# Kernel tuning notes

Hardware: AMD Instinct MI355X
Metric: run time of the kernel (lower is better)

## Reference

```python
import jax, jax.numpy as jnp
import numpy as np

C = 1024  # channel dim
T = 2048  # max context / actual seq len
B = 8

def setup_inputs() -> dict:
    key = jax.random.key(0)
    k1, k2, k3 = jax.random.split(key, 3)
    x = jax.random.normal(k1, (B, T, C), dtype=jnp.float32)
    # torch nn.Linear(C, 3C, bias=False): y = x @ W.T, W shape [3C, C].
    # We store the pre-transposed [C, 3C] / [C, C] matrices for clean matmuls.
    scale = 1.0 / np.sqrt(C)
    Wqkv = jax.random.normal(k2, (C, 3 * C), dtype=jnp.float32) * scale
    Wproj = jax.random.normal(k3, (C, C), dtype=jnp.float32) * scale
    return {"x": x, "Wqkv": Wqkv, "Wproj": Wproj}

def reference(x, Wqkv, Wproj):
    t = x.shape[1]
    qkv = x @ Wqkv                      # [B, t, 3C]
    q, k, v = jnp.split(qkv, 3, axis=-1)  # each [B, t, C]
    w = jnp.einsum('btc,bsc->bts', q, k) * (C ** -0.5)  # [B, t, t]
    causal = jnp.triu(jnp.ones((t, t), dtype=bool), k=1)
    w = jnp.where(causal, -jnp.inf, w)
    a = jax.nn.softmax(w, axis=-1)      # [B, t, t]
    out = jnp.einsum('bts,bsc->btc', a, v)  # [B, t, C]
    return out @ Wproj
```

## Files before the change

### kernel.cpp

```cpp
#include <hip/hip_runtime.h>

typedef unsigned short u16;
typedef __attribute__((ext_vector_type(8))) short bf16x8;
typedef __attribute__((ext_vector_type(4))) float f32x4;

__device__ __forceinline__ u16 f2bf(float f) {
    unsigned u = __float_as_uint(f);
    u += 0x7fffu + ((u >> 16) & 1u);
    return (u16)(u >> 16);
}

__device__ __forceinline__ void g2l16(const void* g, void* l) {
    __builtin_amdgcn_global_load_lds((const __attribute__((address_space(1))) void*)g,
                                     (__attribute__((address_space(3))) void*)l, 16, 0, 0);
}

#define SPACK_ELEMS 2228224LL

#define BM 128
#define BN 128
#define BK 64

template <bool OUT_BF16>
__global__ __launch_bounds__(256, 4) void gemm_bt(
    const u16* __restrict__ A, const u16* __restrict__ B, void* __restrict__ Cout,
    int K, int lda, int ldb, int ldc,
    long long sA, long long sB, long long sC,
    float alpha, int mode)
{
    int bx, by;
    const int bz = blockIdx.z;
    if (mode == 1) {
        int l = blockIdx.x;
        by = (int)((sqrtf(8.f * (float)l + 1.f) - 1.f) * 0.5f);
        while ((by + 1) * (by + 2) / 2 <= l) ++by;
        while (by * (by + 1) / 2 > l) --by;
        bx = l - by * (by + 1) / 2;
    } else if (mode == 2) {
        bx = blockIdx.x; by = (int)gridDim.y - 1 - (int)blockIdx.y;
    } else {
        bx = blockIdx.x; by = blockIdx.y;
    }
    int Keff = K;
    if (mode == 2) { int cap = (by + 1) * BM; if (cap < Keff) Keff = cap; }

    __shared__ alignas(16) u16 As[BM * BK];
    __shared__ alignas(16) u16 Bs[BN * BK];

    const int tid  = threadIdx.x;
    const int wave = tid >> 6, lane = tid & 63;
    const int wm = wave >> 1, wn = wave & 1;
    const int q = lane >> 4, r = lane & 15;

    const long long Pby = 16384LL * (by * (by + 1) / 2);

    const u16* Ab;
    int lda_e = lda;
    if (mode == 2) {
        lda_e = 2 * (by + 1) * BM;
        Ab = A + sA * bz + 2 * Pby;
    } else {
        Ab = A + sA * bz + (size_t)(by * BM) * lda_e;
    }
    const u16* Bb = B + sB * bz + (size_t)(bx * BN) * ldb;

    const u16* ap[4]; const u16* bp[4]; int sb[4];
#pragma unroll
    for (int j = 0; j < 4; ++j) {
        int s   = (wave * 4 + j) * 64 + lane;
        int row = s >> 3;
        int cc  = (s & 7) ^ (row & 7);
        ap[j] = Ab + (size_t)row * lda_e + cc * 8;
        bp[j] = Bb + (size_t)row * ldb + cc * 8;
        sb[j] = (wave * 4 + j) * 64;
    }

    f32x4 acc[4][4] = {};

    const int kiters = Keff / BK;
    for (int kt = 0; kt < kiters; ++kt) {
#pragma unroll
        for (int j = 0; j < 4; ++j) { g2l16(ap[j], As + (size_t)sb[j] * 8); ap[j] += BK; }
#pragma unroll
        for (int j = 0; j < 4; ++j) { g2l16(bp[j], Bs + (size_t)sb[j] * 8); bp[j] += BK; }
        __syncthreads();
#pragma unroll
        for (int ks = 0; ks < 2; ++ks) {
            bf16x8 af[4], bfv[4];
#pragma unroll
            for (int i = 0; i < 4; ++i) {
                int mr = wm * 64 + i * 16 + r;
                int cc = (ks * 4 + q) ^ (mr & 7);
                af[i] = *(const bf16x8*)(As + mr * BK + cc * 8);
            }
#pragma unroll
            for (int i = 0; i < 4; ++i) {
                int nr = wn * 64 + i * 16 + r;
                int cc = (ks * 4 + q) ^ (nr & 7);
                bfv[i] = *(const bf16x8*)(Bs + nr * BK + cc * 8);
            }
#pragma unroll
            for (int i = 0; i < 4; ++i)
#pragma unroll
                for (int jn = 0; jn < 4; ++jn)
                    acc[i][jn] = __builtin_amdgcn_mfma_f32_16x16x32_bf16(
                        af[i], bfv[jn], acc[i][jn], 0, 0, 0);
        }
        __syncthreads();
    }

    if (mode == 1) {
        float* Cp = (float*)Cout + sC * bz + Pby;
        const int ldrow = (by + 1) * BM;
#pragma unroll
        for (int i = 0; i < 4; ++i) {
            int lr = wm * 64 + i * 16 + q * 4;
#pragma unroll
            for (int jn = 0; jn < 4; ++jn) {
                int col = bx * BN + wn * 64 + jn * 16 + r;
#pragma unroll
                for (int rr = 0; rr < 4; ++rr)
                    Cp[(size_t)(lr + rr) * ldrow + col] = acc[i][jn][rr] * alpha;
            }
        }
    } else if constexpr (OUT_BF16) {
        u16* Cp = (u16*)Cout + sC * bz;
#pragma unroll
        for (int i = 0; i < 4; ++i) {
            int rowb = by * BM + wm * 64 + i * 16 + q * 4;
#pragma unroll
            for (int jn = 0; jn < 4; ++jn) {
                int col = bx * BN + wn * 64 + jn * 16 + r;
#pragma unroll
                for (int rr = 0; rr < 4; ++rr)
                    Cp[(size_t)(rowb + rr) * ldc + col] = f2bf(acc[i][jn][rr] * alpha);
            }
        }
    } else {
        float* Cp = (float*)Cout + sC * bz;
#pragma unroll
        for (int i = 0; i < 4; ++i) {
            int rowb = by * BM + wm * 64 + i * 16 + q * 4;
#pragma unroll
            for (int jn = 0; jn < 4; ++jn) {
                int col = bx * BN + wn * 64 + jn * 16 + r;
#pragma unroll
                for (int rr = 0; rr < 4; ++rr)
                    Cp[(size_t)(rowb + rr) * ldc + col] = acc[i][jn][rr] * alpha;
            }
        }
    }
}

__global__ void cast_f32_bf16(const float4* __restrict__ in, ushort4* __restrict__ out) {
    int i = blockIdx.x * 256 + threadIdx.x;
    float4 f = in[i];
    ushort4 o;
    o.x = f2bf(f.x); o.y = f2bf(f.y); o.z = f2bf(f.z); o.w = f2bf(f.w);
    out[i] = o;
}

__global__ void transpose_cast_f32(const float* __restrict__ in, u16* __restrict__ out,
                                   int R, int Cc) {
    __shared__ u16 tile[32][33];
    int tx = threadIdx.x, ty = threadIdx.y;
    int c0 = blockIdx.x * 32, r0 = blockIdx.y * 32;
#pragma unroll
    for (int k = 0; k < 4; ++k)
        tile[ty + k * 8][tx] = f2bf(in[(size_t)(r0 + ty + k * 8) * Cc + c0 + tx]);
    __syncthreads();
#pragma unroll
    for (int k = 0; k < 4; ++k)
        out[(size_t)(c0 + ty + k * 8) * R + r0 + tx] = tile[tx][ty + k * 8];
}

__global__ __launch_bounds__(256) void softmax_causal_packed(
    float* __restrict__ S, long long sS)
{
    const int wave = threadIdx.x >> 6, lane = threadIdx.x & 63;
    const int t = blockIdx.x * 4 + wave;
    const int by = t >> 7, lr = t & 127;
    const int L = (by + 1) << 7;
    float* row = S + (long long)blockIdx.y * sS
               + 16384LL * (by * (by + 1) / 2) + (size_t)lr * L;
    const int n = t + 1;
    const int nit = (L + 255) >> 8;

    float v[32];
    float m = -1e30f;
    for (int it = 0; it < nit; ++it) {
        int c = it * 64 + lane;
        int e = c * 4;
        float4 f = make_float4(-1e30f, -1e30f, -1e30f, -1e30f);
        if (e < n) f = ((const float4*)row)[c];
        v[it * 4 + 0] = (e + 0 < n) ? f.x : -1e30f;
        v[it * 4 + 1] = (e + 1 < n) ? f.y : -1e30f;
        v[it * 4 + 2] = (e + 2 < n) ? f.z : -1e30f;
        v[it * 4 + 3] = (e + 3 < n) ? f.w : -1e30f;
        m = fmaxf(m, fmaxf(fmaxf(v[it * 4 + 0], v[it * 4 + 1]),
                           fmaxf(v[it * 4 + 2], v[it * 4 + 3])));
    }
    for (int off = 32; off > 0; off >>= 1) m = fmaxf(m, __shfl_xor(m, off));

    float s = 0.f;
    for (int it = 0; it < nit; ++it) {
#pragma unroll
        for (int j = 0; j < 4; ++j) {
            v[it * 4 + j] = __expf(v[it * 4 + j] - m);
            s += v[it * 4 + j];
        }
    }
    for (int off = 32; off > 0; off >>= 1) s += __shfl_xor(s, off);
    float inv = 1.f / s;

    u16* orow = (u16*)row;
    for (int it = 0; it < nit; ++it) {
        int c = it * 64 + lane;
        if (c * 4 < L) {
            ushort4 o;
            o.x = f2bf(v[it * 4 + 0] * inv);
            o.y = f2bf(v[it * 4 + 1] * inv);
            o.z = f2bf(v[it * 4 + 2] * inv);
            o.w = f2bf(v[it * 4 + 3] * inv);
            ((ushort4*)orow)[c] = o;
        }
    }
}

extern "C" void kernel_launch(void* const* d_in, const int* in_sizes, int n_in,
                              void* d_out, int out_size, void* d_ws, size_t ws_size,
                              hipStream_t stream)
{
    const float* x     = (const float*)d_in[0];
    const float* Wqkv  = (const float*)d_in[1];
    const float* Wproj = (const float*)d_in[2];
    float* out = (float*)d_out;

    const int Bb = 8, T = 2048, C1 = 1024, C3 = 3072;

    char* ws = (char*)d_ws;
    u16*  xb     = (u16*)(ws);
    u16*  VWpT   = (u16*)(ws);
    u16*  WqkvT  = (u16*)(ws +  33554432ULL);
    u16*  WprojT = (u16*)(ws +  39845888ULL);
    u16*  qkvb   = (u16*)(ws +  41943040ULL);
    float* Sbuf  = (float*)(ws + 142606336ULL);

    const unsigned long long sbytes = SPACK_ELEMS * 4ULL;
    int zc = 1;
    if      (ws_size >= 142606336ULL + 8ULL * sbytes) zc = 8;
    else if (ws_size >= 142606336ULL + 4ULL * sbytes) zc = 4;
    else if (ws_size >= 142606336ULL + 2ULL * sbytes) zc = 2;

    cast_f32_bf16<<<16384, 256, 0, stream>>>((const float4*)x, (ushort4*)xb);

    transpose_cast_f32<<<dim3(96, 32), dim3(32, 8), 0, stream>>>(Wqkv,  WqkvT,  C1, C3);
    transpose_cast_f32<<<dim3(32, 32), dim3(32, 8), 0, stream>>>(Wproj, WprojT, C1, C1);

    gemm_bt<true><<<dim3(24, 128, 1), 256, 0, stream>>>(
        xb, WqkvT, qkvb, C1, C1, C1, C3, 0, 0, 0, 1.0f, 0);

    gemm_bt<true><<<dim3(16, 8, 8), 256, 0, stream>>>(
        WprojT, qkvb + 2 * C1, VWpT, C1, C1, C3, T,
        0, (long long)T * C3, (long long)C1 * T, 1.0f, 0);

    for (int i = 0; i < Bb; i += zc) {
        const u16* qb   = qkvb + (long long)i * T * C3;
        const u16* kb   = qb + C1;
        const u16* vwpb = VWpT + (long long)i * C1 * T;
        float* ob = out + (long long)i * T * C1;

        gemm_bt<false><<<dim3(136, 1, zc), 256, 0, stream>>>(
            qb, kb, Sbuf, C1, C3, C3, 0,
            (long long)T * C3, (long long)T * C3, SPACK_ELEMS,
            0.03125f, 1);

        softmax_causal_packed<<<dim3(T / 4, zc), 256, 0, stream>>>(
            Sbuf, SPACK_ELEMS);

        gemm_bt<false><<<dim3(8, 16, zc), 256, 0, stream>>>(
            (const u16*)Sbuf, vwpb, ob, T, 0, T, C1,
            2LL * SPACK_ELEMS, (long long)C1 * T, (long long)T * C1,
            1.0f, 2);
    }

    (void)in_sizes; (void)n_in; (void)out_size;
}
```

Baseline: 431.6 us.

## Add 256x256-tile 8-wave pipelined GEMM for QKV and V·Wproj projections

Adds a new bf16 GEMM kernel with 256x256 output tiles, 512 threads, double-buffered direct global-to-LDS loads, a fine-grained interleave of LDS reads, global staging and MFMA with explicit waitcnt/barrier control, and setprio around MFMA bursts. The QKV projection and the V×Wproj precompute now use it instead of the 128x128 kernel, aiming for more reuse per loaded byte and better overlap of loads with matrix math. Fewer blocks (768 and 256) may underfill the GPU's CUs, and the heavy manual scheduling depends on the compiler honouring the ordering and on register pressure at 2 blocks per CU.

```diff
diff --git a/kernel.cpp b/kernel.cpp
--- a/kernel.cpp
+++ b/kernel.cpp
@@ -152,6 +152,152 @@
     }
 }
 
+#define GBM 256
+#define GBN 256
+#define GBK 64
+
+__global__ __launch_bounds__(512, 2) void gemm256_bt(
+    const u16* __restrict__ A, const u16* __restrict__ B, u16* __restrict__ Cout,
+    int K, int lda, int ldb, int ldc,
+    long long sA, long long sB, long long sC)
+{
+    const int bx = blockIdx.x, by = blockIdx.y, bz = blockIdx.z;
+
+    __shared__ alignas(16) u16 As[2][GBM * GBK];
+    __shared__ alignas(16) u16 Bs[2][GBN * GBK];
+
+    const int tid  = threadIdx.x;
+    const int wave = tid >> 6, lane = tid & 63;
+    const int wm = wave >> 2, wn = wave & 3;
+    const int q = lane >> 4, r = lane & 15;
+
+    const u16* Ab = A + sA * bz + (size_t)(by * GBM) * lda;
+    const u16* Bb = B + sB * bz + (size_t)(bx * GBN) * ldb;
+
+    const u16* ap[2][2]; const u16* bp[2][2];
+#pragma unroll
+    for (int h = 0; h < 2; ++h)
+#pragma unroll
+        for (int l = 0; l < 2; ++l) {
+            int s   = l * 512 + tid;
+            int row = h * 128 + (s >> 3);
+            int cc  = (s & 7) ^ (row & 7);
+            ap[h][l] = Ab + (size_t)row * lda + cc * 8;
+            bp[h][l] = Bb + (size_t)row * ldb + cc * 8;
+        }
+
+#define STAGE_A(buf, h)                                                        \
+    { g2l16(ap[h][0], &As[buf][((h) * 1024 + 0 * 512 + wave * 64) * 8]);       \
+      ap[h][0] += GBK;                                                         \
+      g2l16(ap[h][1], &As[buf][((h) * 1024 + 1 * 512 + wave * 64) * 8]);       \
+      ap[h][1] += GBK; }
+#define STAGE_B(buf, h)                                                        \
+    { g2l16(bp[h][0], &Bs[buf][((h) * 1024 + 0 * 512 + wave * 64) * 8]);       \
+      bp[h][0] += GBK;                                                         \
+      g2l16(bp[h][1], &Bs[buf][((h) * 1024 + 1 * 512 + wave * 64) * 8]);       \
+      bp[h][1] += GBK; }
+
+    bf16x8 a[4][2], b0[2][2], b1[2][2];
+    f32x4 acc[8][4] = {};
+
+#define G_LDA(mh, buf)                                                         \
+    { _Pragma("unroll") for (int m = 0; m < 4; ++m)                            \
+      _Pragma("unroll") for (int ks = 0; ks < 2; ++ks) {                       \
+          int rw = wm * 128 + (mh) * 64 + m * 16 + r;                          \
+          int cc = (ks * 4 + q) ^ (r & 7);                                     \
+          a[m][ks] = *(const bf16x8*)(&As[buf][rw * GBK + cc * 8]);            \
+      } }
+#define G_LDB(nh, breg, buf)                                                   \
+    { _Pragma("unroll") for (int n = 0; n < 2; ++n)                            \
+      _Pragma("unroll") for (int ks = 0; ks < 2; ++ks) {                       \
+          int rw = wn * 64 + (nh) * 32 + n * 16 + r;                           \
+          int cc = (ks * 4 + q) ^ (r & 7);                                     \
+          breg[n][ks] = *(const bf16x8*)(&Bs[buf][rw * GBK + cc * 8]);         \
+      } }
+#define MFMA16(mh, nh, breg)                                                   \
+    { __builtin_amdgcn_s_setprio(1);                                          \
+      _Pragma("unroll") for (int m = 0; m < 4; ++m)                            \
+      _Pragma("unroll") for (int n = 0; n < 2; ++n)                            \
+      _Pragma("unroll") for (int ks = 0; ks < 2; ++ks)                         \
+          acc[(mh) * 4 + m][(nh) * 2 + n] =                                    \
+              __builtin_amdgcn_mfma_f32_16x16x32_bf16(                         \
+                  a[m][ks], breg[n][ks], acc[(mh) * 4 + m][(nh) * 2 + n],      \
+                  0, 0, 0);                                                    \
+      __builtin_amdgcn_s_setprio(0); }
+
+#define BARR                                                                   \
+    { asm volatile("" ::: "memory");                                           \
+      __builtin_amdgcn_s_barrier();                                            \
+      asm volatile("" ::: "memory"); }
+#define WLGKM asm volatile("s_waitcnt lgkmcnt(0)" ::: "memory")
+#define WVM4 asm volatile("s_waitcnt vmcnt(4)" ::: "memory")
+#define WVM0 asm volatile("s_waitcnt vmcnt(0)" ::: "memory")
+
+    STAGE_B(0, 0); STAGE_B(0, 1);
+    STAGE_A(0, 0); STAGE_A(0, 1);
+    STAGE_B(1, 0); STAGE_B(1, 1);
+    WVM4;
+    BARR;
+
+    const int niter = K / (2 * GBK);
+    for (int i = 0; i < niter - 1; ++i) {
+        G_LDA(0, 0); G_LDB(0, b0, 0); STAGE_A(1, 0);
+        BARR; WLGKM; MFMA16(0, 0, b0); BARR;
+        G_LDB(1, b1, 0); STAGE_A(1, 1);
+        BARR; WLGKM; MFMA16(0, 1, b1); BARR;
+        G_LDA(1, 0); STAGE_B(0, 0);
+        BARR; WLGKM; MFMA16(1, 0, b0); BARR;
+        STAGE_B(0, 1); WVM4;
+        BARR; MFMA16(1, 1, b1); BARR;
+        G_LDA(0, 1); G_LDB(0, b0, 1); STAGE_A(0, 0);
+        BARR; WLGKM; MFMA16(0, 0, b0); BARR;
+        G_LDB(1, b1, 1); STAGE_A(0, 1);
+        BARR; WLGKM; MFMA16(0, 1, b1); BARR;
+        G_LDA(1, 1); STAGE_B(1, 0);
+        BARR; WLGKM; MFMA16(1, 0, b0); BARR;
+        STAGE_B(1, 1); WVM4;
+        BARR; MFMA16(1, 1, b1); BARR;
+    }
+
+    G_LDA(0, 0); G_LDB(0, b0, 0); STAGE_A(1, 0);
+    BARR; WLGKM; MFMA16(0, 0, b0); BARR;
+    G_LDB(1, b1, 0); STAGE_A(1, 1);
+    BARR; WLGKM; MFMA16(0, 1, b1); BARR;
+    G_LDA(1, 0);
+    BARR; WLGKM; MFMA16(1, 0, b0); BARR;
+    WVM0;
+    BARR; MFMA16(1, 1, b1); BARR;
+    G_LDA(0, 1); G_LDB(0, b0, 1);
+    BARR; WLGKM; MFMA16(0, 0, b0); BARR;
+    G_LDB(1, b1, 1);
+    BARR; WLGKM; MFMA16(0, 1, b1); BARR;
+    G_LDA(1, 1);
+    BARR; WLGKM; MFMA16(1, 0, b0); BARR;
+    MFMA16(1, 1, b1);
+
+    u16* Cp = Cout + sC * bz;
+#pragma unroll
+    for (int mf = 0; mf < 8; ++mf) {
+        int rowb = by * GBM + wm * 128 + mf * 16 + q * 4;
+#pragma unroll
+        for (int nf = 0; nf < 4; ++nf) {
+            int col = bx * GBN + wn * 64 + nf * 16 + r;
+#pragma unroll
+            for (int rr = 0; rr < 4; ++rr)
+                Cp[(size_t)(rowb + rr) * ldc + col] = f2bf(acc[mf][nf][rr]);
+        }
+    }
+#undef STAGE_A
+#undef STAGE_B
+#undef G_LDA
+#undef G_LDB
+#undef MFMA16
+#undef BARR
+#undef WLGKM
+#undef WVM4
+#undef WVM0
+}
+
 __global__ void cast_f32_bf16(const float4* __restrict__ in, ushort4* __restrict__ out) {
     int i = blockIdx.x * 256 + threadIdx.x;
     float4 f = in[i];
@@ -257,12 +403,12 @@
     transpose_cast_f32<<<dim3(96, 32), dim3(32, 8), 0, stream>>>(Wqkv,  WqkvT,  C1, C3);
     transpose_cast_f32<<<dim3(32, 32), dim3(32, 8), 0, stream>>>(Wproj, WprojT, C1, C1);
 
-    gemm_bt<true><<<dim3(24, 128, 1), 256, 0, stream>>>(
-        xb, WqkvT, qkvb, C1, C1, C1, C3, 0, 0, 0, 1.0f, 0);
-
-    gemm_bt<true><<<dim3(16, 8, 8), 256, 0, stream>>>(
+    gemm256_bt<<<dim3(12, 64, 1), 512, 0, stream>>>(
+        xb, WqkvT, qkvb, C1, C1, C1, C3, 0, 0, 0);
+
+    gemm256_bt<<<dim3(8, 4, 8), 512, 0, stream>>>(
         WprojT, qkvb + 2 * C1, VWpT, C1, C1, C3, T,
-        0, (long long)T * C3, (long long)C1 * T, 1.0f, 0);
+        0, (long long)T * C3, (long long)C1 * T);
 
     for (int i = 0; i < Bb; i += zc) {
         const u16* qb   = qkvb + (long long)i * T * C3;
```

Measured after the change: 444.9 us. 3.1% more time.
